# Kernel optimization log

Hardware: AMD Instinct MI355X
Metric: run time of the kernel (lower is better)

## Reference

```python
import jax, jax.numpy as jnp
import numpy as np


def setup_inputs() -> dict:
    key = jax.random.key(0)
    k1, k2 = jax.random.split(key)
    B, C, H, W = 32, 256, 64, 64
    data = jax.random.normal(k1, (B, C, H, W), dtype=jnp.float32)
    offset = jax.random.normal(k2, (B, 2, H, W), dtype=jnp.float32)
    trans_std = jnp.float32(0.005)  # learned scalar Parameter
    return {"data": data, "offset": offset, "trans_std": trans_std}


def reference(data, offset, trans_std):
    """Offset-driven bilinear interpolation sampling + global average pooling.

    data:   [B, C, H, W]
    offset: [B, 2, H, W]  (dy, dx) displacement field, scaled by trans_std
    Returns pooled features [B, C].
    """
    B, C, H, W = data.shape
    ts = jnp.clip(trans_std, 0.001, 0.01)  # forward clamps trans_std to [0.001, 0.01]

    # sampling coordinates: base grid + scaled offsets (offsets normalized by H/W)
    ii = jnp.arange(H, dtype=data.dtype)[:, None]   # [H,1]
    jj = jnp.arange(W, dtype=data.dtype)[None, :]   # [1,W]
    y = jnp.clip(ii + ts * offset[:, 0] * H, 0.0, H - 1)  # [B,H,W]
    x = jnp.clip(jj + ts * offset[:, 1] * W, 0.0, W - 1)  # [B,H,W]

    y0 = jnp.clip(jnp.floor(y).astype(jnp.int32), 0, H - 2)
    x0 = jnp.clip(jnp.floor(x).astype(jnp.int32), 0, W - 2)
    y1 = y0 + 1
    x1 = x0 + 1
    wy = y - y0.astype(data.dtype)  # [B,H,W] in [0,1]
    wx = x - x0.astype(data.dtype)

    def sample_one(d, yy0, yy1, xx0, xx1):
        # d: [C,H,W]; index maps: [H,W] -> gathered [C,H,W]
        v00 = d[:, yy0, xx0]
        v01 = d[:, yy0, xx1]
        v10 = d[:, yy1, xx0]
        v11 = d[:, yy1, xx1]
        return v00, v01, v10, v11

    v00, v01, v10, v11 = jax.vmap(sample_one)(data, y0, y1, x0, x1)  # each [B,C,H,W]

    wy_ = wy[:, None]  # broadcast over channels -> [B,1,H,W]
    wx_ = wx[:, None]
    sampled = ((1 - wy_) * (1 - wx_) * v00 + (1 - wy_) * wx_ * v01
               + wy_ * (1 - wx_) * v10 + wy_ * wx_ * v11)  # [B,C,H,W]

    # pooling: global average over spatial locations -> [B,C]
    return jnp.mean(sampled, axis=(2, 3))
```

## Files before the change

### kernel.cpp

```cpp
#include <hip/hip_runtime.h>

#define BATCH 32
#define CHAN  256
#define HGT   64
#define WID   64
#define HW    4096

__global__ __launch_bounds__(256) void weight_map_kernel(
        const float* __restrict__ offset,
        const float* __restrict__ ts_ptr,
        float* __restrict__ A)
{
    const int b   = blockIdx.x;
    const int tid = threadIdx.x;

    __shared__ float acc[HW];
    for (int k = tid; k < HW; k += 256) acc[k] = 0.0f;
    __syncthreads();

    float ts = ts_ptr[0];
    ts = fminf(fmaxf(ts, 0.001f), 0.01f);

    const float* off_y = offset + (size_t)b * 2 * HW;
    const float* off_x = off_y + HW;

    for (int p = tid; p < HW; p += 256) {
        const int i = p >> 6;
        const int j = p & 63;
        const float dy = off_y[p];
        const float dx = off_x[p];
        float y = fminf(fmaxf((float)i + ts * dy * 64.0f, 0.0f), 63.0f);
        float x = fminf(fmaxf((float)j + ts * dx * 64.0f, 0.0f), 63.0f);
        int y0 = (int)floorf(y); y0 = min(max(y0, 0), HGT - 2);
        int x0 = (int)floorf(x); x0 = min(max(x0, 0), WID - 2);
        const float wy = y - (float)y0;
        const float wx = x - (float)x0;
        const int base = (y0 << 6) + x0;
        atomicAdd(&acc[base],           (1.0f - wy) * (1.0f - wx));
        atomicAdd(&acc[base + 1],       (1.0f - wy) * wx);
        atomicAdd(&acc[base + WID],     wy * (1.0f - wx));
        atomicAdd(&acc[base + WID + 1], wy * wx);
    }
    __syncthreads();

    float* Ab = A + (size_t)b * HW;
    const float s = 1.0f / (float)HW;
    for (int k = tid; k < HW; k += 256) Ab[k] = acc[k] * s;
}

__global__ __launch_bounds__(256) void dot_kernel(
        const float* __restrict__ data,
        const float* __restrict__ A,
        float* __restrict__ out)
{
    __shared__ float As[HW];
    const int tid        = threadIdx.x;
    const int base_plane = blockIdx.x << 2;
    const int b          = base_plane >> 8;

    const float* Ab = A + (size_t)b * HW;
    #pragma unroll
    for (int k = 0; k < 4; ++k) {
        const int idx = k * 1024 + tid * 4;
        *reinterpret_cast<float4*>(&As[idx]) =
            *reinterpret_cast<const float4*>(Ab + idx);
    }
    __syncthreads();

    const int wv   = tid >> 6;
    const int lane = tid & 63;
    const float* plane = data + (size_t)(base_plane + wv) * HW;
    const int o = lane << 2;

    float s0 = 0.0f, s1 = 0.0f, s2 = 0.0f, s3 = 0.0f;

    #pragma unroll
    for (int it = 0; it < 4; ++it) {
        const int idx = it * 1024 + o;
        const float4 d0 = *reinterpret_cast<const float4*>(plane + idx);
        const float4 d1 = *reinterpret_cast<const float4*>(plane + idx + 256);
        const float4 d2 = *reinterpret_cast<const float4*>(plane + idx + 512);
        const float4 d3 = *reinterpret_cast<const float4*>(plane + idx + 768);
        const float4 a0 = *reinterpret_cast<const float4*>(&As[idx]);
        const float4 a1 = *reinterpret_cast<const float4*>(&As[idx + 256]);
        const float4 a2 = *reinterpret_cast<const float4*>(&As[idx + 512]);
        const float4 a3 = *reinterpret_cast<const float4*>(&As[idx + 768]);
        s0 = fmaf(a0.x, d0.x, s0); s0 = fmaf(a0.y, d0.y, s0);
        s0 = fmaf(a0.z, d0.z, s0); s0 = fmaf(a0.w, d0.w, s0);
        s1 = fmaf(a1.x, d1.x, s1); s1 = fmaf(a1.y, d1.y, s1);
        s1 = fmaf(a1.z, d1.z, s1); s1 = fmaf(a1.w, d1.w, s1);
        s2 = fmaf(a2.x, d2.x, s2); s2 = fmaf(a2.y, d2.y, s2);
        s2 = fmaf(a2.z, d2.z, s2); s2 = fmaf(a2.w, d2.w, s2);
        s3 = fmaf(a3.x, d3.x, s3); s3 = fmaf(a3.y, d3.y, s3);
        s3 = fmaf(a3.z, d3.z, s3); s3 = fmaf(a3.w, d3.w, s3);
    }

    float s = (s0 + s1) + (s2 + s3);

    #pragma unroll
    for (int off = 32; off > 0; off >>= 1)
        s += __shfl_down(s, off, 64);

    if (lane == 0) out[base_plane + wv] = s;
}

extern "C" void kernel_launch(void* const* d_in, const int* in_sizes, int n_in,
                              void* d_out, int out_size, void* d_ws, size_t ws_size,
                              hipStream_t stream) {
    const float* data   = (const float*)d_in[0];
    const float* offset = (const float*)d_in[1];
    const float* ts     = (const float*)d_in[2];

    float* A   = (float*)d_ws;
    float* out = (float*)d_out;

    weight_map_kernel<<<BATCH, 256, 0, stream>>>(offset, ts, A);
    dot_kernel<<<(BATCH * CHAN) / 4, 256, 0, stream>>>(data, A, out);
}
```

Measured before the change: 214.1 us.

## Fuse weight-map construction into dot kernel, recomputing per block

Merges the two kernels into one: every block rebuilds its batch's bilinear weight map in shared memory via atomics, then dots it with data planes. Data loads are issued into registers before the atomic phase so global latency overlaps the weight-map work. This removes the poorly parallel 32-block weight-map launch and the global round trip of the map, at the cost of redundant per-block recomputation and higher register pressure.

```diff
diff --git a/kernel.cpp b/kernel.cpp
--- a/kernel.cpp
+++ b/kernel.cpp
@@ -6,16 +6,28 @@
 #define WID   64
 #define HW    4096
 
-__global__ __launch_bounds__(256) void weight_map_kernel(
+__global__ __launch_bounds__(256, 4) void fused_kernel(
+        const float* __restrict__ data,
         const float* __restrict__ offset,
         const float* __restrict__ ts_ptr,
-        float* __restrict__ A)
+        float* __restrict__ out)
 {
-    const int b   = blockIdx.x;
-    const int tid = threadIdx.x;
+    __shared__ float A[HW];
+    const int tid        = threadIdx.x;
+    const int base_plane = blockIdx.x << 2;
+    const int b          = base_plane >> 8;
+    const int wv         = tid >> 6;
+    const int lane       = tid & 63;
 
-    __shared__ float acc[HW];
-    for (int k = tid; k < HW; k += 256) acc[k] = 0.0f;
+    const float* plane = data + (size_t)(base_plane + wv) * HW;
+    const int o = lane << 2;
+    float4 d[16];
+    #pragma unroll
+    for (int k = 0; k < 16; ++k)
+        d[k] = *reinterpret_cast<const float4*>(plane + k * 256 + o);
+
+    #pragma unroll
+    for (int k = 0; k < 16; ++k) A[k * 256 + tid] = 0.0f;
     __syncthreads();
 
     float ts = ts_ptr[0];
@@ -24,7 +36,9 @@
     const float* off_y = offset + (size_t)b * 2 * HW;
     const float* off_x = off_y + HW;
 
-    for (int p = tid; p < HW; p += 256) {
+    #pragma unroll
+    for (int it = 0; it < 16; ++it) {
+        const int p = it * 256 + tid;
         const int i = p >> 6;
         const int j = p & 63;
         const float dy = off_y[p];
@@ -36,72 +50,36 @@
         const float wy = y - (float)y0;
         const float wx = x - (float)x0;
         const int base = (y0 << 6) + x0;
-        atomicAdd(&acc[base],           (1.0f - wy) * (1.0f - wx));
-        atomicAdd(&acc[base + 1],       (1.0f - wy) * wx);
-        atomicAdd(&acc[base + WID],     wy * (1.0f - wx));
-        atomicAdd(&acc[base + WID + 1], wy * wx);
+        atomicAdd(&A[base],           (1.0f - wy) * (1.0f - wx));
+        atomicAdd(&A[base + 1],       (1.0f - wy) * wx);
+        atomicAdd(&A[base + WID],     wy * (1.0f - wx));
+        atomicAdd(&A[base + WID + 1], wy * wx);
     }
     __syncthreads();
 
-    float* Ab = A + (size_t)b * HW;
-    const float s = 1.0f / (float)HW;
-    for (int k = tid; k < HW; k += 256) Ab[k] = acc[k] * s;
-}
-
-__global__ __launch_bounds__(256) void dot_kernel(
-        const float* __restrict__ data,
-        const float* __restrict__ A,
-        float* __restrict__ out)
-{
-    __shared__ float As[HW];
-    const int tid        = threadIdx.x;
-    const int base_plane = blockIdx.x << 2;
-    const int b          = base_plane >> 8;
-
-    const float* Ab = A + (size_t)b * HW;
+    float s0 = 0.0f, s1 = 0.0f, s2 = 0.0f, s3 = 0.0f;
     #pragma unroll
-    for (int k = 0; k < 4; ++k) {
-        const int idx = k * 1024 + tid * 4;
-        *reinterpret_cast<float4*>(&As[idx]) =
-            *reinterpret_cast<const float4*>(Ab + idx);
+    for (int k = 0; k < 16; k += 4) {
+        const float4 a0 = *reinterpret_cast<const float4*>(&A[(k + 0) * 256 + o]);
+        const float4 a1 = *reinterpret_cast<const float4*>(&A[(k + 1) * 256 + o]);
+        const float4 a2 = *reinterpret_cast<const float4*>(&A[(k + 2) * 256 + o]);
+        const float4 a3 = *reinterpret_cast<const float4*>(&A[(k + 3) * 256 + o]);
+        s0 = fmaf(a0.x, d[k+0].x, s0); s0 = fmaf(a0.y, d[k+0].y, s0);
+        s0 = fmaf(a0.z, d[k+0].z, s0); s0 = fmaf(a0.w, d[k+0].w, s0);
+        s1 = fmaf(a1.x, d[k+1].x, s1); s1 = fmaf(a1.y, d[k+1].y, s1);
+        s1 = fmaf(a1.z, d[k+1].z, s1); s1 = fmaf(a1.w, d[k+1].w, s1);
+        s2 = fmaf(a2.x, d[k+2].x, s2); s2 = fmaf(a2.y, d[k+2].y, s2);
+        s2 = fmaf(a2.z, d[k+2].z, s2); s2 = fmaf(a2.w, d[k+2].w, s2);
+        s3 = fmaf(a3.x, d[k+3].x, s3); s3 = fmaf(a3.y, d[k+3].y, s3);
+        s3 = fmaf(a3.z, d[k+3].z, s3); s3 = fmaf(a3.w, d[k+3].w, s3);
     }
-    __syncthreads();
-
-    const int wv   = tid >> 6;
-    const int lane = tid & 63;
-    const float* plane = data + (size_t)(base_plane + wv) * HW;
-    const int o = lane << 2;
-
-    float s0 = 0.0f, s1 = 0.0f, s2 = 0.0f, s3 = 0.0f;
-
-    #pragma unroll
-    for (int it = 0; it < 4; ++it) {
-        const int idx = it * 1024 + o;
-        const float4 d0 = *reinterpret_cast<const float4*>(plane + idx);
-        const float4 d1 = *reinterpret_cast<const float4*>(plane + idx + 256);
-        const float4 d2 = *reinterpret_cast<const float4*>(plane + idx + 512);
-        const float4 d3 = *reinterpret_cast<const float4*>(plane + idx + 768);
-        const float4 a0 = *reinterpret_cast<const float4*>(&As[idx]);
-        const float4 a1 = *reinterpret_cast<const float4*>(&As[idx + 256]);
-        const float4 a2 = *reinterpret_cast<const float4*>(&As[idx + 512]);
-        const float4 a3 = *reinterpret_cast<const float4*>(&As[idx + 768]);
-        s0 = fmaf(a0.x, d0.x, s0); s0 = fmaf(a0.y, d0.y, s0);
-        s0 = fmaf(a0.z, d0.z, s0); s0 = fmaf(a0.w, d0.w, s0);
-        s1 = fmaf(a1.x, d1.x, s1); s1 = fmaf(a1.y, d1.y, s1);
-        s1 = fmaf(a1.z, d1.z, s1); s1 = fmaf(a1.w, d1.w, s1);
-        s2 = fmaf(a2.x, d2.x, s2); s2 = fmaf(a2.y, d2.y, s2);
-        s2 = fmaf(a2.z, d2.z, s2); s2 = fmaf(a2.w, d2.w, s2);
-        s3 = fmaf(a3.x, d3.x, s3); s3 = fmaf(a3.y, d3.y, s3);
-        s3 = fmaf(a3.z, d3.z, s3); s3 = fmaf(a3.w, d3.w, s3);
-    }
-
     float s = (s0 + s1) + (s2 + s3);
 
     #pragma unroll
     for (int off = 32; off > 0; off >>= 1)
         s += __shfl_down(s, off, 64);
 
-    if (lane == 0) out[base_plane + wv] = s;
+    if (lane == 0) out[base_plane + wv] = s * (1.0f / (float)HW);
 }
 
 extern "C" void kernel_launch(void* const* d_in, const int* in_sizes, int n_in,
@@ -110,10 +88,7 @@
     const float* data   = (const float*)d_in[0];
     const float* offset = (const float*)d_in[1];
     const float* ts     = (const float*)d_in[2];
-
-    float* A   = (float*)d_ws;
     float* out = (float*)d_out;
 
-    weight_map_kernel<<<BATCH, 256, 0, stream>>>(offset, ts, A);
-    dot_kernel<<<(BATCH * CHAN) / 4, 256, 0, stream>>>(data, A, out);
+    fused_kernel<<<(BATCH * CHAN) / 4, 256, 0, stream>>>(data, offset, ts, out);
 }
```

After: 334.6 us. +56.3%, slower.
